# Performance work log

Hardware: AMD Instinct MI355X
Metric: run time of the kernel (lower is better)

## Reference

```python
import jax, jax.numpy as jnp
import numpy as np

EPS = 1e-8


def setup_inputs() -> dict:
    key = jax.random.key(0)
    k1, k2, k3 = jax.random.split(key, 3)
    n_nodes, n_pos, d, n_seg = 50000, 2048, 128, 32
    pred = jax.random.normal(k1, (n_nodes, d), dtype=jnp.float32)
    target = jax.random.normal(k2, (n_pos, d), dtype=jnp.float32)
    target_identifiers = jax.random.randint(k3, (n_pos,), 0, n_seg, dtype=jnp.int64)
    return {
        "pred": pred,
        "target": target,
        "target_identifiers": target_identifiers,
        "num_segments": n_seg,
    }


def reference(pred, target, target_identifiers, num_segments):
    # Pairwise L2 distance: sqrt(||t||^2 - 2 t.p + ||p||^2 + eps)
    # avoids materializing the [n_pos, n_nodes, d] broadcast tensor.
    t2 = jnp.sum(target * target, axis=-1, keepdims=True)          # [n_pos, 1]
    p2 = jnp.sum(pred * pred, axis=-1)                             # [n_nodes]
    cross = jnp.einsum('pd,nd->pn', target, pred)                  # [n_pos, n_nodes]
    sq = jnp.maximum(t2 - 2.0 * cross + p2[None, :], 0.0)
    dist_mat = jnp.sqrt(sq + EPS)                                  # [n_pos, n_nodes]

    # stage1: scatter_mean over target_identifiers (dim=0)
    seg_sum = jax.ops.segment_sum(dist_mat, target_identifiers,
                                  num_segments=num_segments)       # [n_seg, n_nodes]
    counts = jax.ops.segment_sum(jnp.ones((dist_mat.shape[0],), dist_mat.dtype),
                                 target_identifiers, num_segments=num_segments)
    seg_mean = seg_sum / jnp.maximum(counts, 1.0)[:, None]

    # stage2: mean over segments
    return seg_mean.mean(axis=0)                                   # [n_nodes]
```

## Files before the change

kernel.cpp:

```cpp
#include <hip/hip_runtime.h>

#define DIMK 128
#define SLICE_TILES 4
#define NODES_PER_BLOCK 128

typedef __bf16 bf16x8 __attribute__((ext_vector_type(8)));
typedef float  f32x4  __attribute__((ext_vector_type(4)));

__device__ inline unsigned short f32_to_bf16_rne(float f) {
    unsigned u = __float_as_uint(f);
    u += 0x7FFFu + ((u >> 16) & 1u);
    return (unsigned short)(u >> 16);
}


__global__ void pack_all(const float* __restrict__ pred,
                         const float* __restrict__ tgt,
                         unsigned short* __restrict__ pb,
                         unsigned short* __restrict__ tb,
                         float* __restrict__ p2,
                         float* __restrict__ t2,
                         int n_nodes, int n_rows_pad, int n_pos) {
    int wave = threadIdx.x >> 6, lane = threadIdx.x & 63;
    int row = blockIdx.x * 4 + wave;

    const float* src; unsigned short* dst; float* nrm; float scale; int r;
    if (row < n_rows_pad) {
        src = pred + (size_t)min(row, n_nodes - 1) * DIMK;
        dst = pb; nrm = p2; scale = 1.0f; r = row;
    } else {
        int trow = row - n_rows_pad;
        if (trow >= n_pos) return;
        src = tgt + (size_t)trow * DIMK;
        dst = tb; nrm = t2; scale = -2.0f; r = trow;
    }
    int e = lane * 2;
    float2 v = *(const float2*)(src + e);
    unsigned pk = (unsigned)f32_to_bf16_rne(scale * v.x) |
                  ((unsigned)f32_to_bf16_rne(scale * v.y) << 16);
    int tile = r >> 4, col = r & 15;
    int kk = e >> 5, kb = (e >> 3) & 3, j = e & 7;
    size_t off = (size_t)tile * 2048 + kk * 512 + (kb * 16 + col) * 8 + j;
    *(unsigned*)(dst + off) = pk;
    float s = v.x * v.x + v.y * v.y;
#pragma unroll
    for (int o = 1; o < 64; o <<= 1) s += __shfl_xor(s, o, 64);
    if (lane == 0) nrm[r] = s;
}

__global__ void seg_weights(const int* __restrict__ ids,
                            const int* __restrict__ nseg_p,
                            float* __restrict__ wsa, int n_pos) {
    __shared__ int   cnt[256];
    __shared__ float w[256];
    int nseg = nseg_p[0];
    if (nseg > 256) nseg = 256;
    int t = threadIdx.x;
    if (t < nseg) cnt[t] = 0;
    __syncthreads();
    for (int p = t; p < n_pos; p += blockDim.x) atomicAdd(&cnt[ids[p]], 1);
    __syncthreads();
    if (t < nseg) w[t] = 1.0f / ((float)nseg * (float)max(cnt[t], 1));
    __syncthreads();
    for (int p = t; p < n_pos; p += blockDim.x) wsa[p] = w[ids[p]];
}

__global__ __launch_bounds__(256, 6)
void l2dist_main(const unsigned short* __restrict__ pb,
                 const float* __restrict__ p2,
                 const unsigned short* __restrict__ tb,
                 const float* __restrict__ t2g,
                 const float* __restrict__ wg,
                 float* __restrict__ out,
                 int n_nodes) {
    __shared__ __align__(16) unsigned short lbuf[SLICE_TILES][2048];
    __shared__ __align__(16) float t2_lds[SLICE_TILES * 16];
    __shared__ __align__(16) float w_lds[SLICE_TILES * 16];

    const int tid  = threadIdx.x;
    const int lane = tid & 63;
    const int wave = tid >> 6;
    const int col  = lane & 15;
    const int kb   = lane >> 4;
    const int n0   = blockIdx.y * NODES_PER_BLOCK + wave * 32;

    const int pbase = blockIdx.x * SLICE_TILES;
    const unsigned short* sgp = tb + (size_t)pbase * 2048 + wave * 512 + lane * 8;
    unsigned short* ldst = &lbuf[0][0] + wave * 512;
#pragma unroll
    for (int t = 0; t < SLICE_TILES; ++t) {
        __builtin_amdgcn_global_load_lds(
            (const __attribute__((address_space(1))) unsigned int*)(const void*)
                (sgp + (size_t)t * 2048),
            (__attribute__((address_space(3))) unsigned int*)(void*)
                (ldst + t * 2048),
            16, 0, 0);
    }

    if (tid < SLICE_TILES * 16) {
        t2_lds[tid] = t2g[pbase * 16 + tid];
        w_lds[tid]  = wg[pbase * 16 + tid];
    }

    bf16x8 bfrag[2][4];
    float p2g[2];
    const unsigned short* bp = pb + ((size_t)(n0 >> 4)) * 2048 + (size_t)lane * 8;
#pragma unroll
    for (int g = 0; g < 2; ++g) {
#pragma unroll
        for (int kk = 0; kk < 4; ++kk)
            bfrag[g][kk] = *(const bf16x8*)(bp + g * 2048 + kk * 512);
        p2g[g] = p2[n0 + g * 16 + col];
    }

    __syncthreads();

    float acc0 = 0.f, acc1 = 0.f;
#pragma unroll
    for (int t = 0; t < SLICE_TILES; ++t) {
        const int te = (t + wave) & (SLICE_TILES - 1);

        const unsigned short* rb = &lbuf[te][lane * 8];
        bf16x8 a0 = *(const bf16x8*)(rb);
        bf16x8 a1 = *(const bf16x8*)(rb + 512);
        bf16x8 a2 = *(const bf16x8*)(rb + 1024);
        bf16x8 a3 = *(const bf16x8*)(rb + 1536);

        f32x4 t2v = *(const f32x4*)&t2_lds[te * 16 + kb * 4];
        f32x4 wv  = *(const f32x4*)&w_lds[te * 16 + kb * 4];

        f32x4 d0a = t2v + p2g[0];
        f32x4 d1a = t2v + p2g[1];
        f32x4 d0b = {0.f, 0.f, 0.f, 0.f};
        f32x4 d1b = {0.f, 0.f, 0.f, 0.f};
        d0a = __builtin_amdgcn_mfma_f32_16x16x32_bf16(a0, bfrag[0][0], d0a, 0, 0, 0);
        d1a = __builtin_amdgcn_mfma_f32_16x16x32_bf16(a0, bfrag[1][0], d1a, 0, 0, 0);
        d0b = __builtin_amdgcn_mfma_f32_16x16x32_bf16(a2, bfrag[0][2], d0b, 0, 0, 0);
        d1b = __builtin_amdgcn_mfma_f32_16x16x32_bf16(a2, bfrag[1][2], d1b, 0, 0, 0);
        d0a = __builtin_amdgcn_mfma_f32_16x16x32_bf16(a1, bfrag[0][1], d0a, 0, 0, 0);
        d1a = __builtin_amdgcn_mfma_f32_16x16x32_bf16(a1, bfrag[1][1], d1a, 0, 0, 0);
        d0b = __builtin_amdgcn_mfma_f32_16x16x32_bf16(a3, bfrag[0][3], d0b, 0, 0, 0);
        d1b = __builtin_amdgcn_mfma_f32_16x16x32_bf16(a3, bfrag[1][3], d1b, 0, 0, 0);

        f32x4 s0 = d0a + d0b;
        f32x4 s1 = d1a + d1b;
#pragma unroll
        for (int j = 0; j < 4; ++j) {
            acc0 = fmaf(wv[j], __builtin_amdgcn_sqrtf(fmaxf(s0[j], 0.f)), acc0);
            acc1 = fmaf(wv[j], __builtin_amdgcn_sqrtf(fmaxf(s1[j], 0.f)), acc1);
        }
    }

    acc0 += __shfl_xor(acc0, 16, 64);
    acc0 += __shfl_xor(acc0, 32, 64);
    acc1 += __shfl_xor(acc1, 16, 64);
    acc1 += __shfl_xor(acc1, 32, 64);
    if (lane < 16) {
        int na = n0 + col;
        if (na      < n_nodes) atomicAdd(out + na,      acc0);
        if (na + 16 < n_nodes) atomicAdd(out + na + 16, acc1);
    }
}

extern "C" void kernel_launch(void* const* d_in, const int* in_sizes, int n_in,
                              void* d_out, int out_size, void* d_ws, size_t ws_size,
                              hipStream_t stream) {
    const float* pred  = (const float*)d_in[0];
    const float* tgt   = (const float*)d_in[1];
    const int*   ids   = (const int*)d_in[2];
    const int*   nsegp = (const int*)d_in[3];
    float* out = (float*)d_out;

    int n_nodes = in_sizes[0] / DIMK;
    int n_pos   = in_sizes[2];

    int gy = (n_nodes + NODES_PER_BLOCK - 1) / NODES_PER_BLOCK;
    int n_rows_pad = gy * NODES_PER_BLOCK;

    char* ws = (char*)d_ws;
    size_t off_pb = 0;
    size_t off_tb = off_pb + (size_t)n_rows_pad * DIMK * 2;
    size_t off_p2 = off_tb + (size_t)n_pos * DIMK * 2;
    size_t off_t2 = off_p2 + (size_t)n_rows_pad * 4;
    size_t off_w  = off_t2 + (size_t)n_pos * 4;
    unsigned short* pb  = (unsigned short*)(ws + off_pb);
    unsigned short* tb  = (unsigned short*)(ws + off_tb);
    float*          p2  = (float*)(ws + off_p2);
    float*          t2  = (float*)(ws + off_t2);
    float*          wsa = (float*)(ws + off_w);

    int prows = n_rows_pad + n_pos;
    pack_all<<<(prows + 3) / 4, 256, 0, stream>>>(pred, tgt, pb, tb, p2, t2,
                                                  n_nodes, n_rows_pad, n_pos);
    seg_weights<<<1, 1024, 0, stream>>>(ids, nsegp, wsa, n_pos);
    hipMemsetAsync(out, 0, (size_t)out_size * sizeof(float), stream);

    int gx = (n_pos >> 4) / SLICE_TILES;
    dim3 grid(gx, gy);
    l2dist_main<<<grid, 256, 0, stream>>>(pb, p2, tb, t2, wsa, out, n_nodes);
}
```

Measured before the change: 56.15 us.

## Widen node tile to 48 per wave and transpose MFMA operand roles

Each wave now handles 48 nodes (three 16-node groups) instead of 32, so every LDS-loaded target fragment feeds 12 MFMAs instead of 8. The MFMA operands are swapped so nodes map to output rows and targets to columns, which changes the reduction to shuffles across columns and four atomics per lane group. Occupancy is lowered to 3 blocks per SIMD to make room for the extra fragment registers, and the grid in y shrinks. The goal is more reuse of LDS reads per block, at the cost of fewer resident waves and more shuffle work in the reduction.

```diff
diff --git a/kernel.cpp b/kernel.cpp
--- a/kernel.cpp
+++ b/kernel.cpp
@@ -2,7 +2,7 @@
 
 #define DIMK 128
 #define SLICE_TILES 4
-#define NODES_PER_BLOCK 128
+#define NODES_PER_BLOCK 192
 
 typedef __bf16 bf16x8 __attribute__((ext_vector_type(8)));
 typedef float  f32x4  __attribute__((ext_vector_type(4)));
@@ -65,7 +65,7 @@
     for (int p = t; p < n_pos; p += blockDim.x) wsa[p] = w[ids[p]];
 }
 
-__global__ __launch_bounds__(256, 6)
+__global__ __launch_bounds__(256, 3)
 void l2dist_main(const unsigned short* __restrict__ pb,
                  const float* __restrict__ p2,
                  const unsigned short* __restrict__ tb,
@@ -82,7 +82,7 @@
     const int wave = tid >> 6;
     const int col  = lane & 15;
     const int kb   = lane >> 4;
-    const int n0   = blockIdx.y * NODES_PER_BLOCK + wave * 32;
+    const int n0   = blockIdx.y * NODES_PER_BLOCK + wave * 48;
 
     const int pbase = blockIdx.x * SLICE_TILES;
     const unsigned short* sgp = tb + (size_t)pbase * 2048 + wave * 512 + lane * 8;
@@ -102,20 +102,23 @@
         w_lds[tid]  = wg[pbase * 16 + tid];
     }
 
-    bf16x8 bfrag[2][4];
-    float p2g[2];
+    bf16x8 pfrag[3][4];
+    f32x4  p2r[3];
     const unsigned short* bp = pb + ((size_t)(n0 >> 4)) * 2048 + (size_t)lane * 8;
 #pragma unroll
-    for (int g = 0; g < 2; ++g) {
+    for (int g = 0; g < 3; ++g) {
 #pragma unroll
         for (int kk = 0; kk < 4; ++kk)
-            bfrag[g][kk] = *(const bf16x8*)(bp + g * 2048 + kk * 512);
-        p2g[g] = p2[n0 + g * 16 + col];
-    }
-
-    __syncthreads();
-
-    float acc0 = 0.f, acc1 = 0.f;
+            pfrag[g][kk] = *(const bf16x8*)(bp + g * 2048 + kk * 512);
+        p2r[g] = *(const f32x4*)(p2 + n0 + g * 16 + kb * 4);
+    }
+
+    __syncthreads();
+
+    f32x4 acc0 = {0.f,0.f,0.f,0.f};
+    f32x4 acc1 = {0.f,0.f,0.f,0.f};
+    f32x4 acc2 = {0.f,0.f,0.f,0.f};
+
 #pragma unroll
     for (int t = 0; t < SLICE_TILES; ++t) {
         const int te = (t + wave) & (SLICE_TILES - 1);
@@ -126,39 +129,56 @@
         bf16x8 a2 = *(const bf16x8*)(rb + 1024);
         bf16x8 a3 = *(const bf16x8*)(rb + 1536);
 
-        f32x4 t2v = *(const f32x4*)&t2_lds[te * 16 + kb * 4];
-        f32x4 wv  = *(const f32x4*)&w_lds[te * 16 + kb * 4];
-
-        f32x4 d0a = t2v + p2g[0];
-        f32x4 d1a = t2v + p2g[1];
-        f32x4 d0b = {0.f, 0.f, 0.f, 0.f};
-        f32x4 d1b = {0.f, 0.f, 0.f, 0.f};
-        d0a = __builtin_amdgcn_mfma_f32_16x16x32_bf16(a0, bfrag[0][0], d0a, 0, 0, 0);
-        d1a = __builtin_amdgcn_mfma_f32_16x16x32_bf16(a0, bfrag[1][0], d1a, 0, 0, 0);
-        d0b = __builtin_amdgcn_mfma_f32_16x16x32_bf16(a2, bfrag[0][2], d0b, 0, 0, 0);
-        d1b = __builtin_amdgcn_mfma_f32_16x16x32_bf16(a2, bfrag[1][2], d1b, 0, 0, 0);
-        d0a = __builtin_amdgcn_mfma_f32_16x16x32_bf16(a1, bfrag[0][1], d0a, 0, 0, 0);
-        d1a = __builtin_amdgcn_mfma_f32_16x16x32_bf16(a1, bfrag[1][1], d1a, 0, 0, 0);
-        d0b = __builtin_amdgcn_mfma_f32_16x16x32_bf16(a3, bfrag[0][3], d0b, 0, 0, 0);
-        d1b = __builtin_amdgcn_mfma_f32_16x16x32_bf16(a3, bfrag[1][3], d1b, 0, 0, 0);
-
-        f32x4 s0 = d0a + d0b;
-        f32x4 s1 = d1a + d1b;
+        float t2c = t2_lds[te * 16 + col];
+        float wc  = w_lds[te * 16 + col];
+
+        f32x4 c0a = p2r[0] + t2c;
+        f32x4 c1a = p2r[1] + t2c;
+        f32x4 c2a = p2r[2] + t2c;
+        f32x4 c0b = {0.f,0.f,0.f,0.f};
+        f32x4 c1b = {0.f,0.f,0.f,0.f};
+        f32x4 c2b = {0.f,0.f,0.f,0.f};
+        c0a = __builtin_amdgcn_mfma_f32_16x16x32_bf16(pfrag[0][0], a0, c0a, 0, 0, 0);
+        c1a = __builtin_amdgcn_mfma_f32_16x16x32_bf16(pfrag[1][0], a0, c1a, 0, 0, 0);
+        c2a = __builtin_amdgcn_mfma_f32_16x16x32_bf16(pfrag[2][0], a0, c2a, 0, 0, 0);
+        c0b = __builtin_amdgcn_mfma_f32_16x16x32_bf16(pfrag[0][2], a2, c0b, 0, 0, 0);
+        c1b = __builtin_amdgcn_mfma_f32_16x16x32_bf16(pfrag[1][2], a2, c1b, 0, 0, 0);
+        c2b = __builtin_amdgcn_mfma_f32_16x16x32_bf16(pfrag[2][2], a2, c2b, 0, 0, 0);
+        c0a = __builtin_amdgcn_mfma_f32_16x16x32_bf16(pfrag[0][1], a1, c0a, 0, 0, 0);
+        c1a = __builtin_amdgcn_mfma_f32_16x16x32_bf16(pfrag[1][1], a1, c1a, 0, 0, 0);
+        c2a = __builtin_amdgcn_mfma_f32_16x16x32_bf16(pfrag[2][1], a1, c2a, 0, 0, 0);
+        c0b = __builtin_amdgcn_mfma_f32_16x16x32_bf16(pfrag[0][3], a3, c0b, 0, 0, 0);
+        c1b = __builtin_amdgcn_mfma_f32_16x16x32_bf16(pfrag[1][3], a3, c1b, 0, 0, 0);
+        c2b = __builtin_amdgcn_mfma_f32_16x16x32_bf16(pfrag[2][3], a3, c2b, 0, 0, 0);
+
+        f32x4 s0 = c0a + c0b;
+        f32x4 s1 = c1a + c1b;
+        f32x4 s2 = c2a + c2b;
 #pragma unroll
         for (int j = 0; j < 4; ++j) {
-            acc0 = fmaf(wv[j], __builtin_amdgcn_sqrtf(fmaxf(s0[j], 0.f)), acc0);
-            acc1 = fmaf(wv[j], __builtin_amdgcn_sqrtf(fmaxf(s1[j], 0.f)), acc1);
+            acc0[j] = fmaf(wc, __builtin_amdgcn_sqrtf(fmaxf(s0[j], 0.f)), acc0[j]);
+            acc1[j] = fmaf(wc, __builtin_amdgcn_sqrtf(fmaxf(s1[j], 0.f)), acc1[j]);
+            acc2[j] = fmaf(wc, __builtin_amdgcn_sqrtf(fmaxf(s2[j], 0.f)), acc2[j]);
         }
     }
 
-    acc0 += __shfl_xor(acc0, 16, 64);
-    acc0 += __shfl_xor(acc0, 32, 64);
-    acc1 += __shfl_xor(acc1, 16, 64);
-    acc1 += __shfl_xor(acc1, 32, 64);
-    if (lane < 16) {
-        int na = n0 + col;
-        if (na      < n_nodes) atomicAdd(out + na,      acc0);
-        if (na + 16 < n_nodes) atomicAdd(out + na + 16, acc1);
+#pragma unroll
+    for (int m = 1; m <= 8; m <<= 1) {
+#pragma unroll
+        for (int j = 0; j < 4; ++j) {
+            acc0[j] += __shfl_xor(acc0[j], m, 64);
+            acc1[j] += __shfl_xor(acc1[j], m, 64);
+            acc2[j] += __shfl_xor(acc2[j], m, 64);
+        }
+    }
+    if (col == 0) {
+        int nb = n0 + kb * 4;
+#pragma unroll
+        for (int j = 0; j < 4; ++j) {
+            if (nb + j      < n_nodes) atomicAdd(out + nb + j,      acc0[j]);
+            if (nb + 16 + j < n_nodes) atomicAdd(out + nb + 16 + j, acc1[j]);
+            if (nb + 32 + j < n_nodes) atomicAdd(out + nb + 32 + j, acc2[j]);
+        }
     }
 }
 
```

Result: slower. 71.11 us (+26.6%).
